# Performance work log

Measured on AMD Instinct MI355X. Metric: run time of the kernel, lower is better.

Reference implementation:

```python
import jax, jax.numpy as jnp
import numpy as np

N_HEADS = 16

def setup_inputs() -> dict:
    key = jax.random.key(0)
    k0, k1, k2 = jax.random.split(key, 3)
    B, T, C = 4, 2048, 1024
    x = jax.random.normal(k0, (B, T, C), dtype=jnp.float32)
    # nn.Linear params: y = x @ W.T + b
    w_qkv = jax.random.normal(k1, (3 * C, C), dtype=jnp.float32) * 0.02
    b_qkv = jnp.zeros((3 * C,), dtype=jnp.float32)
    w_proj = jax.random.normal(k2, (C, C), dtype=jnp.float32) * 0.02
    b_proj = jnp.zeros((C,), dtype=jnp.float32)
    return {"x": x, "w_qkv": w_qkv, "b_qkv": b_qkv, "w_proj": w_proj, "b_proj": b_proj}

def reference(x, w_qkv, b_qkv, w_proj, b_proj):
    B, T, C = x.shape
    H = N_HEADS
    hd = C // H
    qkv = x @ w_qkv.T + b_qkv                      # [B, T, 3C]
    q, k, v = jnp.split(qkv, 3, axis=-1)           # each [B, T, C]
    q = q.reshape(B, T, H, hd).transpose(0, 2, 1, 3)  # [B, H, T, hd]
    k = k.reshape(B, T, H, hd).transpose(0, 2, 1, 3)
    v = v.reshape(B, T, H, hd).transpose(0, 2, 1, 3)
    # note: original scales by emb_dim**-0.5 (C), not head_dim**-0.5
    wei = jnp.einsum("bhqd,bhkd->bhqk", q, k) * (C ** -0.5)  # [B, H, T, T]
    causal = jnp.tril(jnp.ones((T, T), dtype=bool))
    wei = jnp.where(causal, wei, -jnp.inf)
    att = jax.nn.softmax(wei, axis=-1)
    out = jnp.einsum("bhqk,bhkd->bhqd", att, v)    # [B, H, T, hd]
    out = out.transpose(0, 2, 1, 3).reshape(B, T, C)
    return out @ w_proj.T + b_proj
```

## Files before the change

kernel.cpp:

```cpp
#include <hip/hip_runtime.h>
#include <hip/hip_bf16.h>

typedef __bf16 bf16;
typedef __bf16 bf16x8 __attribute__((ext_vector_type(8)));
typedef __bf16 bf16x4 __attribute__((ext_vector_type(4)));
typedef float  f32x4  __attribute__((ext_vector_type(4)));
typedef short  short4_t __attribute__((ext_vector_type(4)));

#define LDS_ASYNC16(g, l)                                            \
  __builtin_amdgcn_global_load_lds(                                  \
      (const __attribute__((address_space(1))) void*)(g),            \
      (__attribute__((address_space(3))) void*)(l), 16, 0, 0)

#define QSCALE 0.04508421995f

__global__ void cvt3_f32_bf16(const float* __restrict__ i0, bf16* __restrict__ o0, int n0,
                              const float* __restrict__ i1, bf16* __restrict__ o1, int n1,
                              const float* __restrict__ i2, bf16* __restrict__ o2, int n2) {
  int i = blockIdx.x * blockDim.x + threadIdx.x;
  const float* in;
  bf16* out;
  if (i < n0) {
    in = i0; out = o0;
  } else if (i < n0 + n1) {
    i -= n0; in = i1; out = o1;
  } else {
    i -= n0 + n1;
    if (i >= n2) return;
    in = i2; out = o2;
  }
  float4 v = ((const float4*)in)[i];
  bf16x4 o = {(bf16)v.x, (bf16)v.y, (bf16)v.z, (bf16)v.w};
  ((bf16x4*)out)[i] = o;
}

template <int MODE>
__global__ __launch_bounds__(256) void gemm_bt(
    const bf16* __restrict__ A, const bf16* __restrict__ B,
    const float* __restrict__ bias, float* __restrict__ outf,
    bf16* __restrict__ oq, bf16* __restrict__ ok, bf16* __restrict__ ov,
    int M, int N, int K) {
  __shared__ bf16 As[2][128 * 32];
  __shared__ bf16 Bs[2][128 * 32];
  const int tid = threadIdx.x;
  const int wave = tid >> 6, lane = tid & 63;
  const int quad = lane >> 4, l15 = lane & 15;
  const int bm = blockIdx.x * 128, bn = blockIdx.y * 128;
  const int wrow = (wave >> 1) << 6, wcol = (wave & 1) << 6;
  const int srow = tid >> 2;
  const int schunk = (tid & 3) * 8;

  f32x4 acc[4][4] = {};

  const bf16* ga0 = A + (size_t)(bm + srow) * K + schunk;
  const bf16* ga1 = A + (size_t)(bm + srow + 64) * K + schunk;
  const bf16* gb0 = B + (size_t)(bn + srow) * K + schunk;
  const bf16* gb1 = B + (size_t)(bn + srow + 64) * K + schunk;
  char* lA = (char*)As + wave * 1024;
  char* lB = (char*)Bs + wave * 1024;

  for (int k0 = 0; k0 < K; k0 += 64) {
    __syncthreads();
    LDS_ASYNC16(ga0 + k0, lA);
    LDS_ASYNC16(ga1 + k0, lA + 4096);
    LDS_ASYNC16(gb0 + k0, lB);
    LDS_ASYNC16(gb1 + k0, lB + 4096);
    LDS_ASYNC16(ga0 + k0 + 32, lA + 8192);
    LDS_ASYNC16(ga1 + k0 + 32, lA + 8192 + 4096);
    LDS_ASYNC16(gb0 + k0 + 32, lB + 8192);
    LDS_ASYNC16(gb1 + k0 + 32, lB + 8192 + 4096);
    __syncthreads();
#pragma unroll
    for (int s = 0; s < 2; ++s) {
      bf16x8 af[4], bfr[4];
#pragma unroll
      for (int mi = 0; mi < 4; ++mi)
        af[mi] = *(const bf16x8*)&As[s][(wrow + mi * 16 + l15) * 32 + quad * 8];
#pragma unroll
      for (int ni = 0; ni < 4; ++ni)
        bfr[ni] = *(const bf16x8*)&Bs[s][(wcol + ni * 16 + l15) * 32 + quad * 8];
#pragma unroll
      for (int mi = 0; mi < 4; ++mi)
#pragma unroll
        for (int ni = 0; ni < 4; ++ni)
          acc[mi][ni] = __builtin_amdgcn_mfma_f32_16x16x32_bf16(
              af[mi], bfr[ni], acc[mi][ni], 0, 0, 0);
    }
  }

#pragma unroll
  for (int mi = 0; mi < 4; ++mi) {
    const int row0 = bm + wrow + mi * 16 + quad * 4;
#pragma unroll
    for (int ni = 0; ni < 4; ++ni) {
      const int col = bn + wcol + ni * 16 + l15;
      const float bv = bias[col];
      if (MODE == 0) {
#pragma unroll
        for (int r = 0; r < 4; ++r)
          outf[(size_t)(row0 + r) * N + col] = acc[mi][ni][r] + bv;
      } else {
        const int part = col >> 10;
        const int cn = col & 1023, h = cn >> 6, d = cn & 63;
        const int b = row0 >> 11, t0 = row0 & 2047;
        if (part == 2) {
          bf16x4 pk = {(bf16)(acc[mi][ni][0] + bv), (bf16)(acc[mi][ni][1] + bv),
                       (bf16)(acc[mi][ni][2] + bv), (bf16)(acc[mi][ni][3] + bv)};
          *(bf16x4*)(ov + ((size_t)(b * 16 + h) * 64 + d) * 2048 + t0) = pk;
        } else {
          const float sc = part ? 1.0f : QSCALE;
          bf16* dst = (part ? ok : oq) + ((size_t)(b * 16 + h) * 2048 + t0) * 64 + d;
#pragma unroll
          for (int r = 0; r < 4; ++r)
            dst[(size_t)r * 64] = (bf16)((acc[mi][ni][r] + bv) * sc);
        }
      }
    }
  }
}

__global__ __launch_bounds__(256) void flash_attn(
    const bf16* __restrict__ qb, const bf16* __restrict__ kb,
    const bf16* __restrict__ vt, bf16* __restrict__ ob) {
  constexpr int T = 2048;
  __shared__ bf16 Ks[2][64 * 72];
  __shared__ bf16 Vs[2][64 * 72];
  __shared__ float Ls[4][2][4][16];
  const int tid = threadIdx.x, wave = tid >> 6, lane = tid & 63;
  const int quad = lane >> 4, l15 = lane & 15;
  const int bh = blockIdx.x;
  const int b = bh >> 4, h = bh & 15;
  const bf16* qbase = qb + (size_t)bh * T * 64;
  const bf16* kbase = kb + (size_t)bh * T * 64;
  const bf16* vbase = vt + (size_t)bh * 64 * T;
  const int srow = tid >> 3, sc = (tid & 7) * 8;

#pragma unroll 1
  for (int half = 0; half < 2; ++half) {
    const int qt = half ? (15 - (int)blockIdx.y) : (int)blockIdx.y;
    const int q0 = qt * 128 + wave * 32;

    bf16x8 qf[2][2];
#pragma unroll
    for (int qi = 0; qi < 2; ++qi)
#pragma unroll
      for (int ks = 0; ks < 2; ++ks)
        qf[qi][ks] = *(const bf16x8*)(qbase + (size_t)(q0 + qi * 16 + l15) * 64 +
                                      ks * 32 + quad * 8);

    f32x4 lsumv[2] = {};
    f32x4 oacc[2][4] = {};

    const int nkt = 2 * qt + 2;
    const int ktp = q0 >> 6;

    {
      uint4 k0 = *(const uint4*)(kbase + (size_t)srow * 64 + sc);
      uint4 k1 = *(const uint4*)(kbase + (size_t)(srow + 32) * 64 + sc);
      uint4 v0 = *(const uint4*)(vbase + (size_t)srow * T + sc);
      uint4 v1 = *(const uint4*)(vbase + (size_t)(srow + 32) * T + sc);
      *(uint4*)&Ks[0][srow * 72 + sc] = k0;
      *(uint4*)&Ks[0][(srow + 32) * 72 + sc] = k1;
      *(uint4*)&Vs[0][srow * 72 + sc] = v0;
      *(uint4*)&Vs[0][(srow + 32) * 72 + sc] = v1;
    }

#pragma unroll 1
    for (int kt = 0; kt < nkt; ++kt) {
      __syncthreads();
      const int cur = kt & 1;
      const bool pre = (kt + 1) < nkt;
      uint4 pk0, pk1, pv0, pv1;
      if (pre) {
        const bf16* kp = kbase + (size_t)(kt + 1) * 64 * 64;
        const bf16* vp = vbase + (kt + 1) * 64;
        pk0 = *(const uint4*)(kp + (size_t)srow * 64 + sc);
        pk1 = *(const uint4*)(kp + (size_t)(srow + 32) * 64 + sc);
        pv0 = *(const uint4*)(vp + (size_t)srow * T + sc);
        pv1 = *(const uint4*)(vp + (size_t)(srow + 32) * T + sc);
      }
      if (kt <= ktp) {
        f32x4 st[4][2];
#pragma unroll
        for (int ki = 0; ki < 4; ++ki) {
          bf16x8 kfa = *(const bf16x8*)&Ks[cur][(ki * 16 + l15) * 72 + quad * 8];
          bf16x8 kfb =
              *(const bf16x8*)&Ks[cur][(ki * 16 + l15) * 72 + 32 + quad * 8];
#pragma unroll
          for (int qi = 0; qi < 2; ++qi) {
            f32x4 a = {0.f, 0.f, 0.f, 0.f};
            a = __builtin_amdgcn_mfma_f32_16x16x32_bf16(kfa, qf[qi][0], a, 0, 0, 0);
            a = __builtin_amdgcn_mfma_f32_16x16x32_bf16(kfb, qf[qi][1], a, 0, 0, 0);
            st[ki][qi] = a;
          }
        }
        if (kt == ktp) {
#pragma unroll
          for (int ki = 0; ki < 4; ++ki)
#pragma unroll
            for (int qi = 0; qi < 2; ++qi)
#pragma unroll
              for (int r = 0; r < 4; ++r) {
                const int kcol = kt * 64 + ki * 16 + quad * 4 + r;
                const int qrow = q0 + qi * 16 + l15;
                if (kcol > qrow) st[ki][qi][r] = -__builtin_inff();
              }
        }
        short4_t pa[4][2];
#pragma unroll
        for (int ki = 0; ki < 4; ++ki)
#pragma unroll
          for (int qi = 0; qi < 2; ++qi) {
#pragma unroll
            for (int r = 0; r < 4; ++r)
              st[ki][qi][r] = __builtin_amdgcn_exp2f(st[ki][qi][r]);
            lsumv[qi] += st[ki][qi];
            bf16x4 pk = {(bf16)st[ki][qi][0], (bf16)st[ki][qi][1],
                         (bf16)st[ki][qi][2], (bf16)st[ki][qi][3]};
            pa[ki][qi] = __builtin_bit_cast(short4_t, pk);
          }
#pragma unroll
        for (int di = 0; di < 4; ++di)
#pragma unroll
          for (int ki = 0; ki < 4; ++ki) {
            bf16x4 vv = *(const bf16x4*)&Vs[cur][(di * 16 + l15) * 72 +
                                               ki * 16 + quad * 4];
            short4_t vb = __builtin_bit_cast(short4_t, vv);
#pragma unroll
            for (int qi = 0; qi < 2; ++qi)
              oacc[qi][di] = __builtin_amdgcn_mfma_f32_16x16x16bf16_1k(
                  pa[ki][qi], vb, oacc[qi][di], 0, 0, 0);
          }
      }
      if (pre) {
        const int nxt = cur ^ 1;
        *(uint4*)&Ks[nxt][srow * 72 + sc] = pk0;
        *(uint4*)&Ks[nxt][(srow + 32) * 72 + sc] = pk1;
        *(uint4*)&Vs[nxt][srow * 72 + sc] = pv0;
        *(uint4*)&Vs[nxt][(srow + 32) * 72 + sc] = pv1;
      }
    }

#pragma unroll
    for (int qi = 0; qi < 2; ++qi)
      Ls[wave][qi][quad][l15] =
          lsumv[qi][0] + lsumv[qi][1] + lsumv[qi][2] + lsumv[qi][3];
#pragma unroll
    for (int qi = 0; qi < 2; ++qi)
#pragma unroll
      for (int r = 0; r < 4; ++r) {
        const int rloc = quad * 4 + r;
        const float l = Ls[wave][qi][0][rloc] + Ls[wave][qi][1][rloc] +
                        Ls[wave][qi][2][rloc] + Ls[wave][qi][3][rloc];
        const float inv = 1.f / l;
        const int t = q0 + qi * 16 + rloc;
#pragma unroll
        for (int di = 0; di < 4; ++di) {
          const int d = di * 16 + l15;
          ob[((size_t)b * 2048 + t) * 1024 + h * 64 + d] =
              (bf16)(oacc[qi][di][r] * inv);
        }
      }
  }
}

extern "C" void kernel_launch(void* const* d_in, const int* in_sizes, int n_in,
                              void* d_out, int out_size, void* d_ws,
                              size_t ws_size, hipStream_t stream) {
  const float* x = (const float*)d_in[0];
  const float* w_qkv = (const float*)d_in[1];
  const float* b_qkv = (const float*)d_in[2];
  const float* w_proj = (const float*)d_in[3];
  const float* b_proj = (const float*)d_in[4];
  float* out = (float*)d_out;

  const int B = 4, T = 2048, C = 1024;
  const size_t nx = (size_t)B * T * C;

  char* ws = (char*)d_ws;
  bf16* xb = (bf16*)ws;      ws += nx * 2;
  bf16* wqkvb = (bf16*)ws;   ws += (size_t)3 * C * C * 2;
  bf16* wprojb = (bf16*)ws;  ws += (size_t)C * C * 2;
  bf16* qb = (bf16*)ws;      ws += nx * 2;
  bf16* kbuf = (bf16*)ws;    ws += nx * 2;
  bf16* vtb = (bf16*)ws;     ws += nx * 2;
  bf16* attb = (bf16*)ws;    ws += nx * 2;

  const int n0 = (int)(nx / 4), n1 = 3 * C * C / 4, n2 = C * C / 4;
  cvt3_f32_bf16<<<(n0 + n1 + n2 + 255) / 256, 256, 0, stream>>>(
      x, xb, n0, w_qkv, wqkvb, n1, w_proj, wprojb, n2);

  dim3 g1(64, 24);
  gemm_bt<1><<<g1, 256, 0, stream>>>(xb, wqkvb, b_qkv, nullptr, qb, kbuf, vtb,
                                     B * T, 3 * C, C);
  dim3 g2(64, 8);
  flash_attn<<<g2, 256, 0, stream>>>(qb, kbuf, vtb, attb);

  dim3 g3(64, 8);
  gemm_bt<0><<<g3, 256, 0, stream>>>(attb, wprojb, b_proj, out, nullptr,
                                     nullptr, nullptr, B * T, C, C);
}
```

Measured before the change: 252.6 us.

## Shrink flash-attention query tile to 64 rows and double grid

Each block now handles 64-row query tiles (16 rows per wave) instead of 128, with paired causal tiles indexed from 31 down, and the grid's y dimension is doubled to 16. This removes the masked-out wasted iterations per wave (the `kt <= ktp` skip) and gives more blocks for occupancy and load balance. The cost is that K/V tiles are loaded from global memory twice as often per query row, and each wave does less MFMA work per LDS read. A barrier is added before the first K/V LDS fill of each half.

After: 264.7 us. 4.8% more time.

```diff
diff --git a/kernel.cpp b/kernel.cpp
--- a/kernel.cpp
+++ b/kernel.cpp
@@ -125,7 +125,7 @@
   constexpr int T = 2048;
   __shared__ bf16 Ks[2][64 * 72];
   __shared__ bf16 Vs[2][64 * 72];
-  __shared__ float Ls[4][2][4][16];
+  __shared__ float Ls[4][4][16];
   const int tid = threadIdx.x, wave = tid >> 6, lane = tid & 63;
   const int quad = lane >> 4, l15 = lane & 15;
   const int bh = blockIdx.x;
@@ -137,23 +137,21 @@
 
 #pragma unroll 1
   for (int half = 0; half < 2; ++half) {
-    const int qt = half ? (15 - (int)blockIdx.y) : (int)blockIdx.y;
-    const int q0 = qt * 128 + wave * 32;
-
-    bf16x8 qf[2][2];
-#pragma unroll
-    for (int qi = 0; qi < 2; ++qi)
-#pragma unroll
-      for (int ks = 0; ks < 2; ++ks)
-        qf[qi][ks] = *(const bf16x8*)(qbase + (size_t)(q0 + qi * 16 + l15) * 64 +
-                                      ks * 32 + quad * 8);
-
-    f32x4 lsumv[2] = {};
-    f32x4 oacc[2][4] = {};
-
-    const int nkt = 2 * qt + 2;
-    const int ktp = q0 >> 6;
-
+    const int qt = half ? (31 - (int)blockIdx.y) : (int)blockIdx.y;
+    const int q0 = qt * 64 + wave * 16;
+
+    bf16x8 qf[2];
+#pragma unroll
+    for (int ks = 0; ks < 2; ++ks)
+      qf[ks] = *(const bf16x8*)(qbase + (size_t)(q0 + l15) * 64 + ks * 32 +
+                                quad * 8);
+
+    f32x4 lsumv = {};
+    f32x4 oacc[4] = {};
+
+    const int nkt = qt + 1;
+
+    __syncthreads();
     {
       uint4 k0 = *(const uint4*)(kbase + (size_t)srow * 64 + sc);
       uint4 k1 = *(const uint4*)(kbase + (size_t)(srow + 32) * 64 + sc);
@@ -179,59 +177,48 @@
         pv0 = *(const uint4*)(vp + (size_t)srow * T + sc);
         pv1 = *(const uint4*)(vp + (size_t)(srow + 32) * T + sc);
       }
-      if (kt <= ktp) {
-        f32x4 st[4][2];
+      f32x4 st[4];
+#pragma unroll
+      for (int ki = 0; ki < 4; ++ki) {
+        bf16x8 kfa = *(const bf16x8*)&Ks[cur][(ki * 16 + l15) * 72 + quad * 8];
+        bf16x8 kfb =
+            *(const bf16x8*)&Ks[cur][(ki * 16 + l15) * 72 + 32 + quad * 8];
+        f32x4 a = {0.f, 0.f, 0.f, 0.f};
+        a = __builtin_amdgcn_mfma_f32_16x16x32_bf16(kfa, qf[0], a, 0, 0, 0);
+        a = __builtin_amdgcn_mfma_f32_16x16x32_bf16(kfb, qf[1], a, 0, 0, 0);
+        st[ki] = a;
+      }
+      if (kt == qt) {
+#pragma unroll
+        for (int ki = 0; ki < 4; ++ki)
+#pragma unroll
+          for (int r = 0; r < 4; ++r) {
+            const int kcol = kt * 64 + ki * 16 + quad * 4 + r;
+            const int qrow = q0 + l15;
+            if (kcol > qrow) st[ki][r] = -__builtin_inff();
+          }
+      }
+      short4_t pa[4];
+#pragma unroll
+      for (int ki = 0; ki < 4; ++ki) {
+#pragma unroll
+        for (int r = 0; r < 4; ++r)
+          st[ki][r] = __builtin_amdgcn_exp2f(st[ki][r]);
+        lsumv += st[ki];
+        bf16x4 pk = {(bf16)st[ki][0], (bf16)st[ki][1], (bf16)st[ki][2],
+                     (bf16)st[ki][3]};
+        pa[ki] = __builtin_bit_cast(short4_t, pk);
+      }
+#pragma unroll
+      for (int di = 0; di < 4; ++di)
 #pragma unroll
         for (int ki = 0; ki < 4; ++ki) {
-          bf16x8 kfa = *(const bf16x8*)&Ks[cur][(ki * 16 + l15) * 72 + quad * 8];
-          bf16x8 kfb =
-              *(const bf16x8*)&Ks[cur][(ki * 16 + l15) * 72 + 32 + quad * 8];
-#pragma unroll
-          for (int qi = 0; qi < 2; ++qi) {
-            f32x4 a = {0.f, 0.f, 0.f, 0.f};
-            a = __builtin_amdgcn_mfma_f32_16x16x32_bf16(kfa, qf[qi][0], a, 0, 0, 0);
-            a = __builtin_amdgcn_mfma_f32_16x16x32_bf16(kfb, qf[qi][1], a, 0, 0, 0);
-            st[ki][qi] = a;
-          }
+          bf16x4 vv = *(const bf16x4*)&Vs[cur][(di * 16 + l15) * 72 + ki * 16 +
+                                              quad * 4];
+          short4_t vb = __builtin_bit_cast(short4_t, vv);
+          oacc[di] = __builtin_amdgcn_mfma_f32_16x16x16bf16_1k(pa[ki], vb,
+                                                               oacc[di], 0, 0, 0);
         }
-        if (kt == ktp) {
-#pragma unroll
-          for (int ki = 0; ki < 4; ++ki)
-#pragma unroll
-            for (int qi = 0; qi < 2; ++qi)
-#pragma unroll
-              for (int r = 0; r < 4; ++r) {
-                const int kcol = kt * 64 + ki * 16 + quad * 4 + r;
-                const int qrow = q0 + qi * 16 + l15;
-                if (kcol > qrow) st[ki][qi][r] = -__builtin_inff();
-              }
-        }
-        short4_t pa[4][2];
-#pragma unroll
-        for (int ki = 0; ki < 4; ++ki)
-#pragma unroll
-          for (int qi = 0; qi < 2; ++qi) {
-#pragma unroll
-            for (int r = 0; r < 4; ++r)
-              st[ki][qi][r] = __builtin_amdgcn_exp2f(st[ki][qi][r]);
-            lsumv[qi] += st[ki][qi];
-            bf16x4 pk = {(bf16)st[ki][qi][0], (bf16)st[ki][qi][1],
-                         (bf16)st[ki][qi][2], (bf16)st[ki][qi][3]};
-            pa[ki][qi] = __builtin_bit_cast(short4_t, pk);
-          }
-#pragma unroll
-        for (int di = 0; di < 4; ++di)
-#pragma unroll
-          for (int ki = 0; ki < 4; ++ki) {
-            bf16x4 vv = *(const bf16x4*)&Vs[cur][(di * 16 + l15) * 72 +
-                                               ki * 16 + quad * 4];
-            short4_t vb = __builtin_bit_cast(short4_t, vv);
-#pragma unroll
-            for (int qi = 0; qi < 2; ++qi)
-              oacc[qi][di] = __builtin_amdgcn_mfma_f32_16x16x16bf16_1k(
-                  pa[ki][qi], vb, oacc[qi][di], 0, 0, 0);
-          }
-      }
       if (pre) {
         const int nxt = cur ^ 1;
         *(uint4*)&Ks[nxt][srow * 72 + sc] = pk0;
@@ -241,26 +228,21 @@
       }
     }
 
-#pragma unroll
-    for (int qi = 0; qi < 2; ++qi)
-      Ls[wave][qi][quad][l15] =
-          lsumv[qi][0] + lsumv[qi][1] + lsumv[qi][2] + lsumv[qi][3];
-#pragma unroll
-    for (int qi = 0; qi < 2; ++qi)
-#pragma unroll
-      for (int r = 0; r < 4; ++r) {
-        const int rloc = quad * 4 + r;
-        const float l = Ls[wave][qi][0][rloc] + Ls[wave][qi][1][rloc] +
-                        Ls[wave][qi][2][rloc] + Ls[wave][qi][3][rloc];
-        const float inv = 1.f / l;
-        const int t = q0 + qi * 16 + rloc;
-#pragma unroll
-        for (int di = 0; di < 4; ++di) {
-          const int d = di * 16 + l15;
-          ob[((size_t)b * 2048 + t) * 1024 + h * 64 + d] =
-              (bf16)(oacc[qi][di][r] * inv);
-        }
-      }
+    Ls[wave][quad][l15] = lsumv[0] + lsumv[1] + lsumv[2] + lsumv[3];
+#pragma unroll
+    for (int r = 0; r < 4; ++r) {
+      const int rloc = quad * 4 + r;
+      const float l = Ls[wave][0][rloc] + Ls[wave][1][rloc] +
+                      Ls[wave][2][rloc] + Ls[wave][3][rloc];
+      const float inv = 1.f / l;
+      const int t = q0 + rloc;
+#pragma unroll
+      for (int di = 0; di < 4; ++di) {
+        const int d = di * 16 + l15;
+        ob[((size_t)b * 2048 + t) * 1024 + h * 64 + d] =
+            (bf16)(oacc[di][r] * inv);
+      }
+    }
   }
 }
 
@@ -293,7 +275,7 @@
   dim3 g1(64, 24);
   gemm_bt<1><<<g1, 256, 0, stream>>>(xb, wqkvb, b_qkv, nullptr, qb, kbuf, vtb,
                                      B * T, 3 * C, C);
-  dim3 g2(64, 8);
+  dim3 g2(64, 16);
   flash_attn<<<g2, 256, 0, stream>>>(qb, kbuf, vtb, attb);
 
   dim3 g3(64, 8);
```
